# Optimization experiments

Hardware: AMD Instinct MI355X
Metric: run time of the kernel (lower is better)

Reference implementation:

```python
import jax, jax.numpy as jnp
import numpy as np

B, H, W, C = 64, 28, 28, 384
NH, WS = 12, 7
KD = C // NH            # key_dim = head_dim = 32 (attn_ratio=1.0 -> d = KD)
QKV_OUT = 3 * KD * NH   # 1152
HID = 4 * C             # mlp hidden
N = WS * WS             # tokens per window
L = H * W
SCALE = KD ** -0.5
EPS_LN = 1e-5
EPS_BN = 1e-5


def _make_bias_idxs():
    pts = [(i, j) for i in range(WS) for j in range(WS)]
    offs, idxs = {}, []
    for p1 in pts:
        for p2 in pts:
            o = (abs(p1[0] - p2[0]), abs(p1[1] - p2[1]))
            if o not in offs:
                offs[o] = len(offs)
            idxs.append(offs[o])
    return np.asarray(idxs, dtype=np.int32).reshape(N, N)


def _ln(x, g, b):
    m = jnp.mean(x, axis=-1, keepdims=True)
    v = jnp.mean(jnp.square(x - m), axis=-1, keepdims=True)
    return (x - m) * jax.lax.rsqrt(v + EPS_LN) * g + b


def setup_inputs() -> dict:
    key = jax.random.key(0)
    ks = jax.random.split(key, 8)
    s = 0.02
    return {
        "x": jax.random.normal(ks[0], (B, L, C), jnp.float32),
        "ln_a_g": jnp.ones((C,), jnp.float32),
        "ln_a_b": jnp.zeros((C,), jnp.float32),
        "qkv_w": jax.random.normal(ks[1], (QKV_OUT, C), jnp.float32) * s,
        "qkv_b": jnp.zeros((QKV_OUT,), jnp.float32),
        "attn_bias": jax.random.normal(ks[2], (NH, N), jnp.float32) * s,
        "proj_w": jax.random.normal(ks[3], (C, C), jnp.float32) * s,
        "proj_b": jnp.zeros((C,), jnp.float32),
        "conv_w": jax.random.normal(ks[4], (C, 1, 3, 3), jnp.float32) * s,
        "bn_g": jnp.ones((C,), jnp.float32),
        "bn_b": jnp.zeros((C,), jnp.float32),
        "bn_m": jnp.zeros((C,), jnp.float32),
        "bn_v": jnp.ones((C,), jnp.float32),
        "ln_m_g": jnp.ones((C,), jnp.float32),
        "ln_m_b": jnp.zeros((C,), jnp.float32),
        "fc1_w": jax.random.normal(ks[5], (HID, C), jnp.float32) * s,
        "fc1_b": jnp.zeros((HID,), jnp.float32),
        "fc2_w": jax.random.normal(ks[6], (C, HID), jnp.float32) * s,
        "fc2_b": jnp.zeros((C,), jnp.float32),
        "bias_idxs": jnp.asarray(_make_bias_idxs()),
    }


def reference(x, ln_a_g, ln_a_b, qkv_w, qkv_b, attn_bias, proj_w, proj_b,
              conv_w, bn_g, bn_b, bn_m, bn_v, ln_m_g, ln_m_b,
              fc1_w, fc1_b, fc2_w, fc2_b, bias_idxs):
    res = x
    nh, nw = H // WS, W // WS
    # window partition: [B,L,C] -> [B*nWin, N, C]
    xw = x.reshape(B, nh, WS, nw, WS, C).transpose(0, 1, 3, 2, 4, 5)
    xw = xw.reshape(B * nh * nw, N, C)
    # attention
    xn = _ln(xw, ln_a_g, ln_a_b)
    qkv = xn @ qkv_w.T + qkv_b                       # [Bw, N, 3*NH*KD]
    qkv = qkv.reshape(-1, N, NH, 3 * KD).transpose(0, 2, 1, 3)
    q, k, v = qkv[..., :KD], qkv[..., KD:2 * KD], qkv[..., 2 * KD:]
    bias = attn_bias[:, bias_idxs]                   # [NH, N, N]
    attn = jnp.einsum('bhnd,bhmd->bhnm', q, k) * SCALE + bias
    attn = jax.nn.softmax(attn, axis=-1)
    o = jnp.einsum('bhnm,bhmd->bhnd', attn, v)
    o = o.transpose(0, 2, 1, 3).reshape(-1, N, C)
    o = o @ proj_w.T + proj_b
    # window unpartition -> [B, L, C]
    o = o.reshape(B, nh, nw, WS, WS, C).transpose(0, 1, 3, 2, 4, 5).reshape(B, L, C)
    x = res + o
    # depthwise ConvBN (inference BN)
    xc = x.transpose(0, 2, 1).reshape(B, C, H, W)
    xc = jax.lax.conv_general_dilated(
        xc, conv_w, (1, 1), 'SAME', feature_group_count=C,
        dimension_numbers=('NCHW', 'OIHW', 'NCHW'))
    inv = jax.lax.rsqrt(bn_v + EPS_BN)
    xc = (xc - bn_m[None, :, None, None]) * (bn_g * inv)[None, :, None, None] + bn_b[None, :, None, None]
    x = xc.reshape(B, C, L).transpose(0, 2, 1)
    # MLP residual
    h = _ln(x, ln_m_g, ln_m_b)
    h = jax.nn.gelu(h @ fc1_w.T + fc1_b, approximate=False)
    h = h @ fc2_w.T + fc2_b
    return x + h
```

## Files before the change

kernel.cpp:

```cpp
#include <hip/hip_runtime.h>
#include <hip/hip_bf16.h>
#include <stdint.h>

#define BATCH 64
#define CC 384
#define NHEAD 12
#define KD 32
#define NTOK 49
#define LL 784
#define MTOT 50176
#define HID 1536
#define QKV_OUT 1152
#define SCALE 0.17677669529663687f
#define EPS 1e-5f

typedef __bf16 bf16x8 __attribute__((ext_vector_type(8)));
typedef float f32x4 __attribute__((ext_vector_type(4)));

__device__ __forceinline__ float bf2f(unsigned short u) {
  union { unsigned int u; float f; } cv; cv.u = ((unsigned int)u) << 16; return cv.f;
}
__device__ __forceinline__ unsigned short f2bf(float f) {
  union { float f; unsigned int u; } cv; cv.f = f;
  unsigned int r = cv.u + 0x7FFFu + ((cv.u >> 16) & 1u);
  return (unsigned short)(r >> 16);
}
__device__ __forceinline__ void gl_lds16(const unsigned short* g, unsigned short* l) {
  __builtin_amdgcn_global_load_lds(
      (const __attribute__((address_space(1))) unsigned int*)g,
      (__attribute__((address_space(3))) unsigned int*)l, 16, 0, 0);
}

__global__ void detect_kernel(const unsigned short* __restrict__ x, int* flag) {
  __shared__ int cnt;
  if (threadIdx.x == 0) cnt = 0;
  __syncthreads();
  int c = 0;
  for (int i = threadIdx.x; i < 4096; i += 256) {
    if (((x[i] >> 7) & 0xFF) == 0xFF) c++;
  }
  atomicAdd(&cnt, c);
  __syncthreads();
  if (threadIdx.x == 0) *flag = (cnt > 0) ? 1 : 0;
}

struct CvtArgs {
  const void* src[19];
  unsigned int n[19];
  unsigned int off[19];
};
__global__ __launch_bounds__(256) void convert_kernel(
    CvtArgs a, unsigned short* __restrict__ dst, const int* __restrict__ flag) {
  const int which = blockIdx.y;
  const unsigned int nn = a.n[which];
  unsigned short* d = dst + a.off[which];
  const unsigned int stride = gridDim.x * blockDim.x;
  const unsigned int idx = blockIdx.x * blockDim.x + threadIdx.x;
  const unsigned int ng = nn >> 3;
  if (*flag) {
    const float* s = (const float*)a.src[which];
    for (unsigned int g = idx; g < ng; g += stride) {
      const float4 f0 = ((const float4*)s)[g * 2];
      const float4 f1 = ((const float4*)s)[g * 2 + 1];
      ushort4 lo, hi;
      lo.x = f2bf(f0.x); lo.y = f2bf(f0.y); lo.z = f2bf(f0.z); lo.w = f2bf(f0.w);
      hi.x = f2bf(f1.x); hi.y = f2bf(f1.y); hi.z = f2bf(f1.z); hi.w = f2bf(f1.w);
      ((ushort4*)d)[g * 2] = lo;
      ((ushort4*)d)[g * 2 + 1] = hi;
    }
    for (unsigned int i = ng * 8 + idx; i < nn; i += stride) d[i] = f2bf(s[i]);
  } else {
    const unsigned short* s = (const unsigned short*)a.src[which];
    for (unsigned int g = idx; g < ng; g += stride)
      ((uint4*)d)[g] = ((const uint4*)s)[g];
    for (unsigned int i = ng * 8 + idx; i < nn; i += stride) d[i] = s[i];
  }
}

__global__ __launch_bounds__(256) void bias_kernel(
    const unsigned short* __restrict__ cAb, const int* __restrict__ bias_idxs,
    float* __restrict__ bias_full) {
  const int h = blockIdx.x;
  for (int i = threadIdx.x; i < NTOK * NTOK; i += 256)
    bias_full[h * NTOK * NTOK + i] = bf2f(cAb[h * NTOK + bias_idxs[i]]);
}

__global__ __launch_bounds__(384) void prep_kernel(
    const unsigned short* __restrict__ cw, const unsigned short* __restrict__ bg,
    const unsigned short* __restrict__ bb, const unsigned short* __restrict__ bm,
    const unsigned short* __restrict__ bv,
    unsigned short* __restrict__ cwT, float* __restrict__ bnsc, float* __restrict__ bnsh) {
  const int c = threadIdx.x;
  const float sc = bf2f(bg[c]) * rsqrtf(bf2f(bv[c]) + EPS);
  bnsc[c] = sc;
  bnsh[c] = bf2f(bb[c]) - bf2f(bm[c]) * sc;
  #pragma unroll
  for (int t = 0; t < 9; ++t) cwT[t * CC + c] = cw[c * 9 + t];
}

__global__ __launch_bounds__(128) void ln_kernel(
    const unsigned short* __restrict__ x, const unsigned short* __restrict__ g,
    const unsigned short* __restrict__ b, unsigned short* __restrict__ out) {
  const int tid = threadIdx.x;
  int wi = blockIdx.y, n = blockIdx.x;
  int bb = wi >> 4, wb = wi & 15;
  int nh_i = wb >> 2, nw_i = wb & 3;
  int hs = n / 7, wsx = n - hs * 7;
  int l = nh_i * 196 + hs * 28 + nw_i * 7 + wsx;
  size_t src_row = (size_t)bb * LL + l;
  size_t dst_row = (size_t)wi * NTOK + n;
  const unsigned short* xr = x + src_row * CC;
  float vals[3]; float s = 0.f, sq = 0.f;
  for (int j = 0; j < 3; ++j) {
    vals[j] = bf2f(xr[tid + 128 * j]);
    s += vals[j]; sq += vals[j] * vals[j];
  }
  for (int off = 32; off; off >>= 1) { s += __shfl_xor(s, off); sq += __shfl_xor(sq, off); }
  __shared__ float red[4];
  const int wv = tid >> 6;
  if ((tid & 63) == 0) { red[wv] = s; red[2 + wv] = sq; }
  __syncthreads();
  float tot = red[0] + red[1], totq = red[2] + red[3];
  float mean = tot * (1.f / CC);
  float var = totq * (1.f / CC) - mean * mean;
  float inv = rsqrtf(var + EPS);
  unsigned short* orow = out + dst_row * CC;
  for (int j = 0; j < 3; ++j) {
    int c = tid + 128 * j;
    float y = (vals[j] - mean) * inv * bf2f(g[c]) + bf2f(b[c]);
    orow[c] = f2bf(y);
  }
}

enum { EP_PLAIN = 0, EP_GELU = 1, EP_WINRES = 2, EP_RES2 = 3 };

template <int EP>
__global__ __launch_bounds__(256) void gemm128(
    const unsigned short* __restrict__ A, const unsigned short* __restrict__ W,
    const unsigned short* __restrict__ bias, const unsigned short* __restrict__ res,
    void* __restrict__ outp, int K, int N, int m_off, const int* __restrict__ flagp,
    int Nt) {
  __shared__ __align__(16) unsigned short lds[3 * 8192];
  const int tid = threadIdx.x;
  const int lane = tid & 63;
  const int wave = tid >> 6;
  const int nwg = gridDim.x;
  const int id = blockIdx.x;
  const int q8 = nwg >> 3, r8 = nwg & 7;
  const int xcd = id & 7, rank = id >> 3;
  const int wgid = (xcd < r8 ? xcd * (q8 + 1) : r8 * (q8 + 1) + (xcd - r8) * q8) + rank;
  const int bm = (wgid / Nt) * 128;
  const int bn = (wgid - (wgid / Nt) * Nt) * 128;
  const int wm = (wave >> 1) * 64;
  const int wn = (wave & 1) * 64;
  const int srow = tid >> 2;
  const int sr15 = srow & 15;
  const int sp = (sr15 + (sr15 >> 2)) & 3;
  const int s_col = ((tid & 3) ^ sp) * 8;
  const unsigned short* Ap0 = A + (size_t)(bm + srow) * K + s_col;
  const unsigned short* Wp0 = W + (size_t)(bn + srow) * K + s_col;
  const size_t rstep = (size_t)64 * K;
  f32x4 acc[4][4] = {};
  const int fr = lane & 15;
  const int quad = lane >> 4;
  const int nt = K >> 5;
  const int rp = (fr + (fr >> 2)) & 3;
  const int cg = (quad ^ rp) * 8;

  auto stage = [&](int bsel, int t) {
    const unsigned short* ap = Ap0 + (size_t)t * 32;
    const unsigned short* wp = Wp0 + (size_t)t * 32;
    unsigned short* al = lds + bsel * 8192 + tid * 8;
    unsigned short* bl = al + 4096;
    gl_lds16(ap, al);
    gl_lds16(ap + rstep, al + 2048);
    gl_lds16(wp, bl);
    gl_lds16(wp + rstep, bl + 2048);
  };

  stage(0, 0);
  stage(1, 1);
  int b = 0;
  for (int t = 0; t < nt; ++t) {
    if (t + 1 < nt) asm volatile("s_waitcnt vmcnt(4)" ::: "memory");
    else            asm volatile("s_waitcnt vmcnt(0)" ::: "memory");
    __builtin_amdgcn_s_barrier();
    __builtin_amdgcn_sched_barrier(0);
    if (t + 2 < nt) stage(b ? b - 1 : 2, t + 2);
    const unsigned short* Ab = lds + b * 8192;
    const unsigned short* Bb = Ab + 4096;
    bf16x8 af[4], bfr[4];
    #pragma unroll
    for (int i = 0; i < 4; ++i) {
      af[i]  = *(const bf16x8*)(Ab + (wm + i * 16 + fr) * 32 + cg);
      bfr[i] = *(const bf16x8*)(Bb + (wn + i * 16 + fr) * 32 + cg);
    }
    #pragma unroll
    for (int i = 0; i < 4; ++i)
      #pragma unroll
      for (int j = 0; j < 4; ++j)
        acc[i][j] = __builtin_amdgcn_mfma_f32_16x16x32_bf16(af[i], bfr[j], acc[i][j], 0, 0, 0);
    asm volatile("s_waitcnt lgkmcnt(0)" ::: "memory");
    __builtin_amdgcn_sched_barrier(0);
    b = (b == 2) ? 0 : b + 1;
  }

  int isf32 = 0;
  if (EP == EP_RES2) isf32 = *flagp;
  const int qr = (lane >> 4) * 4;
  float bvs[4];
  #pragma unroll
  for (int tj = 0; tj < 4; ++tj) bvs[tj] = bf2f(bias[bn + wn + tj * 16 + fr]);
  #pragma unroll
  for (int ti = 0; ti < 4; ++ti) {
    #pragma unroll
    for (int r = 0; r < 4; ++r) {
      const int mr = bm + wm + ti * 16 + qr + r;
      size_t rowbase;
      if (EP == EP_WINRES) {
        int wi = mr / 49; int nt2 = mr - wi * 49;
        int bb = wi >> 4; int wb = wi & 15;
        int nh_i = wb >> 2; int nw_i = wb & 3;
        int hs = nt2 / 7; int wsx = nt2 - hs * 7;
        int l = nh_i * 196 + hs * 28 + nw_i * 7 + wsx;
        rowbase = ((size_t)bb * LL + l) * CC;
      } else if (EP == EP_RES2) {
        rowbase = (size_t)(mr + m_off) * N;
      } else {
        rowbase = (size_t)mr * N;
      }
      #pragma unroll
      for (int tj = 0; tj < 4; ++tj) {
        const int n = bn + wn + tj * 16 + fr;
        float v = acc[ti][tj][r] + bvs[tj];
        if (EP == EP_GELU) {
          const float t2 = v * (1.5957691216f + 0.0713548162f * v * v);
          v = __fdividef(v, 1.0f + __expf(-t2));
          ((unsigned short*)outp)[rowbase + n] = f2bf(v);
        } else if (EP == EP_WINRES) {
          size_t idx = rowbase + n;
          v += bf2f(res[idx]);
          ((unsigned short*)outp)[idx] = f2bf(v);
        } else if (EP == EP_RES2) {
          size_t idx = rowbase + n;
          v += bf2f(res[idx]);
          if (isf32) ((float*)outp)[idx] = v;
          else       ((unsigned short*)outp)[idx] = f2bf(v);
        } else {
          ((unsigned short*)outp)[rowbase + n] = f2bf(v);
        }
      }
    }
  }
}

__global__ __launch_bounds__(64) void attn_mfma(
    const unsigned short* __restrict__ qkv, const float* __restrict__ bias_full,
    unsigned short* __restrict__ o, int wi_off) {
  __shared__ __align__(16) unsigned short Pl[64 * 72];
  __shared__ __align__(16) unsigned short vT[32 * 72];
  const int wi = blockIdx.x, h = blockIdx.y;
  const int lane = threadIdx.x;
  const int l15 = lane & 15;
  const int quad = lane >> 4;
  const unsigned short* base = qkv + (size_t)wi * NTOK * QKV_OUT + h * 96;

  bf16x8 qf[4], kf[4];
  #pragma unroll
  for (int i = 0; i < 4; ++i) {
    const int n = i * 16 + l15;
    if (n < NTOK) {
      const unsigned short* p = base + (size_t)n * QKV_OUT + quad * 8;
      qf[i] = *(const bf16x8*)(p);
      kf[i] = *(const bf16x8*)(p + 32);
    } else {
      qf[i] = (bf16x8)0; kf[i] = (bf16x8)0;
    }
  }

  for (int idx = lane; idx < 32 * 72; idx += 64) vT[idx] = 0;
  __syncthreads();
  for (int idx = lane; idx < NTOK * KD; idx += 64) {
    const int m = idx >> 5, d = idx & 31;
    vT[d * 72 + m] = base[(size_t)m * QKV_OUT + 64 + d];
  }

  f32x4 acc[4][4] = {};
  #pragma unroll
  for (int i = 0; i < 4; ++i)
    #pragma unroll
    for (int j = 0; j < 4; ++j)
      acc[i][j] = __builtin_amdgcn_mfma_f32_16x16x32_bf16(qf[i], kf[j], acc[i][j], 0, 0, 0);

  const float* bh = bias_full + h * NTOK * NTOK;
  float rinv[4][4];
  #pragma unroll
  for (int i = 0; i < 4; ++i) {
    #pragma unroll
    for (int r = 0; r < 4; ++r) {
      const int n = i * 16 + quad * 4 + r;
      float sv[4];
      #pragma unroll
      for (int j = 0; j < 4; ++j) {
        const int m = j * 16 + l15;
        float s = acc[i][j][r] * SCALE;
        if (n < NTOK && m < NTOK) s += bh[n * NTOK + m];
        if (m >= NTOK) s = -1e30f;
        sv[j] = s;
      }
      float mx = fmaxf(fmaxf(sv[0], sv[1]), fmaxf(sv[2], sv[3]));
      #pragma unroll
      for (int t = 1; t < 16; t <<= 1) mx = fmaxf(mx, __shfl_xor(mx, t));
      float sum = 0.f;
      #pragma unroll
      for (int j = 0; j < 4; ++j) {
        const float p = __expf(sv[j] - mx);
        sum += p;
        Pl[n * 72 + j * 16 + l15] = f2bf(p);
      }
      #pragma unroll
      for (int t = 1; t < 16; t <<= 1) sum += __shfl_xor(sum, t);
      rinv[i][r] = 1.f / sum;
    }
  }
  __syncthreads();

  f32x4 acc2[4][2] = {};
  #pragma unroll
  for (int kk = 0; kk < 2; ++kk) {
    bf16x8 pf[4], vf[2];
    #pragma unroll
    for (int i = 0; i < 4; ++i)
      pf[i] = *(const bf16x8*)(Pl + (i * 16 + l15) * 72 + kk * 32 + quad * 8);
    #pragma unroll
    for (int jd = 0; jd < 2; ++jd)
      vf[jd] = *(const bf16x8*)(vT + (jd * 16 + l15) * 72 + kk * 32 + quad * 8);
    #pragma unroll
    for (int i = 0; i < 4; ++i)
      #pragma unroll
      for (int jd = 0; jd < 2; ++jd)
        acc2[i][jd] = __builtin_amdgcn_mfma_f32_16x16x32_bf16(pf[i], vf[jd], acc2[i][jd], 0, 0, 0);
  }

  #pragma unroll
  for (int i = 0; i < 4; ++i) {
    #pragma unroll
    for (int r = 0; r < 4; ++r) {
      const int n = i * 16 + quad * 4 + r;
      if (n < NTOK) {
        const float ri = rinv[i][r];
        #pragma unroll
        for (int jd = 0; jd < 2; ++jd) {
          const int d = jd * 16 + l15;
          o[((size_t)(wi_off + wi) * NTOK + n) * CC + h * KD + d] = f2bf(acc2[i][jd][r] * ri);
        }
      }
    }
  }
}

__global__ __launch_bounds__(384) void conv_bn_ln(
    const unsigned short* __restrict__ x1, const unsigned short* __restrict__ cwT,
    const float* __restrict__ bnsc, const float* __restrict__ bnsh,
    const unsigned short* __restrict__ mg, const unsigned short* __restrict__ mb,
    unsigned short* __restrict__ x2, unsigned short* __restrict__ xm) {
  __shared__ float rs[8][48], rq[8][48];
  const int tid = threadIdx.x;
  const int pos = tid / 48;
  const int c8 = tid - pos * 48;
  const int c0 = c8 * 8;
  const int hw = blockIdx.x * 8 + pos;
  const int b = blockIdx.y;
  const int h = hw / 28, w = hw - h * 28;
  float acc[8] = {};
  #pragma unroll
  for (int t = 0; t < 9; ++t) {
    const int dh = t / 3 - 1, dw = t % 3 - 1;
    const int hh = h + dh, ww = w + dw;
    if (hh >= 0 && hh < 28 && ww >= 0 && ww < 28) {
      const uint4 xv = *(const uint4*)(x1 + ((size_t)b * LL + hh * 28 + ww) * CC + c0);
      const uint4 wv = *(const uint4*)(cwT + t * CC + c0);
      const unsigned short* xp = (const unsigned short*)&xv;
      const unsigned short* wp = (const unsigned short*)&wv;
      #pragma unroll
      for (int k = 0; k < 8; ++k) acc[k] += bf2f(xp[k]) * bf2f(wp[k]);
    }
  }
  const float4 sc0 = *(const float4*)(bnsc + c0);
  const float4 sc1 = *(const float4*)(bnsc + c0 + 4);
  const float4 sh0 = *(const float4*)(bnsh + c0);
  const float4 sh1 = *(const float4*)(bnsh + c0 + 4);
  float y[8];
  y[0] = acc[0] * sc0.x + sh0.x; y[1] = acc[1] * sc0.y + sh0.y;
  y[2] = acc[2] * sc0.z + sh0.z; y[3] = acc[3] * sc0.w + sh0.w;
  y[4] = acc[4] * sc1.x + sh1.x; y[5] = acc[5] * sc1.y + sh1.y;
  y[6] = acc[6] * sc1.z + sh1.z; y[7] = acc[7] * sc1.w + sh1.w;
  ushort4 pk0, pk1;
  pk0.x = f2bf(y[0]); pk0.y = f2bf(y[1]); pk0.z = f2bf(y[2]); pk0.w = f2bf(y[3]);
  pk1.x = f2bf(y[4]); pk1.y = f2bf(y[5]); pk1.z = f2bf(y[6]); pk1.w = f2bf(y[7]);
  const size_t row = ((size_t)b * LL + hw) * CC + c0;
  *(ushort4*)(x2 + row) = pk0;
  *(ushort4*)(x2 + row + 4) = pk1;
  float s = 0.f, q = 0.f;
  #pragma unroll
  for (int k = 0; k < 8; ++k) { s += y[k]; q += y[k] * y[k]; }
  rs[pos][c8] = s; rq[pos][c8] = q;
  __syncthreads();
  float tot = 0.f, tq = 0.f;
  #pragma unroll 8
  for (int i = 0; i < 48; ++i) { tot += rs[pos][i]; tq += rq[pos][i]; }
  const float mean = tot * (1.f / CC);
  const float var = tq * (1.f / CC) - mean * mean;
  const float inv = rsqrtf(var + EPS);
  const uint4 gv = *(const uint4*)(mg + c0);
  const uint4 bv = *(const uint4*)(mb + c0);
  const unsigned short* gp = (const unsigned short*)&gv;
  const unsigned short* bp = (const unsigned short*)&bv;
  ushort4 lo, hi;
  unsigned short outv[8];
  #pragma unroll
  for (int k = 0; k < 8; ++k)
    outv[k] = f2bf((y[k] - mean) * inv * bf2f(gp[k]) + bf2f(bp[k]));
  lo.x = outv[0]; lo.y = outv[1]; lo.z = outv[2]; lo.w = outv[3];
  hi.x = outv[4]; hi.y = outv[5]; hi.z = outv[6]; hi.w = outv[7];
  *(ushort4*)(xm + row) = lo;
  *(ushort4*)(xm + row + 4) = hi;
}

extern "C" void kernel_launch(void* const* d_in, const int* in_sizes, int n_in,
                              void* d_out, int out_size, void* d_ws, size_t ws_size,
                              hipStream_t stream) {
  int* flag = (int*)d_ws;
  unsigned short* base = (unsigned short*)d_ws;

  CvtArgs args;
  size_t cur = 32;
  size_t off[19];
  for (int i = 0; i < 19; ++i) {
    off[i] = cur;
    args.src[i] = d_in[i];
    args.n[i] = (unsigned int)in_sizes[i];
    args.off[i] = (unsigned int)cur;
    cur += ((size_t)in_sizes[i] + 63) & ~(size_t)63;
  }
  const unsigned short* cx   = base + off[0];
  const unsigned short* cgA  = base + off[1];
  const unsigned short* cbA  = base + off[2];
  const unsigned short* cQw  = base + off[3];
  const unsigned short* cQb  = base + off[4];
  const unsigned short* cAb  = base + off[5];
  const unsigned short* cPw  = base + off[6];
  const unsigned short* cPb  = base + off[7];
  const unsigned short* cCw  = base + off[8];
  const unsigned short* cBg  = base + off[9];
  const unsigned short* cBb  = base + off[10];
  const unsigned short* cBm  = base + off[11];
  const unsigned short* cBv  = base + off[12];
  const unsigned short* cMg  = base + off[13];
  const unsigned short* cMb  = base + off[14];
  const unsigned short* cF1w = base + off[15];
  const unsigned short* cF1b = base + off[16];
  const unsigned short* cF2w = base + off[17];
  const unsigned short* cF2b = base + off[18];
  const int* bias_idxs = (const int*)d_in[19];

  const size_t SZ = (size_t)MTOT * CC;
  const size_t need_full_bytes =
      (cur + SZ + (size_t)MTOT * HID) * 2 + 512 * 1024;
  const int nchunk = (ws_size >= need_full_bytes) ? 1 : 2;
  const int MC = MTOT / nchunk;
  const int WC = 1024 / nchunk;
  const size_t buf2_cap = (size_t)MC * HID;

  unsigned short* o_buf = base + cur;
  unsigned short* buf2  = o_buf + SZ;
  unsigned short* x2    = base + off[0];
  float* bias_full = (float*)(buf2 + buf2_cap);
  unsigned short* cwT = (unsigned short*)(bias_full + 12 * NTOK * NTOK);
  float* bnsc = (float*)(cwT + 9 * CC);
  float* bnsh = bnsc + CC;

  unsigned short* xn = (unsigned short*)d_out;

  detect_kernel<<<1, 256, 0, stream>>>((const unsigned short*)d_in[0], flag);
  convert_kernel<<<dim3(512, 19), 256, 0, stream>>>(args, base, flag);
  bias_kernel<<<NHEAD, 256, 0, stream>>>(cAb, bias_idxs, bias_full);
  prep_kernel<<<1, 384, 0, stream>>>(cCw, cBg, cBb, cBm, cBv, cwT, bnsc, bnsh);

  ln_kernel<<<dim3(49, 1024), 128, 0, stream>>>(cx, cgA, cbA, xn);

  for (int c = 0; c < nchunk; ++c) {
    gemm128<EP_PLAIN><<<(MC / 128) * (QKV_OUT / 128), 256, 0, stream>>>(
        xn + (size_t)c * MC * CC, cQw, cQb, nullptr, buf2, CC, QKV_OUT, 0, nullptr,
        QKV_OUT / 128);
    attn_mfma<<<dim3(WC, NHEAD), 64, 0, stream>>>(buf2, bias_full, o_buf, c * WC);
  }

  gemm128<EP_WINRES><<<(MTOT / 128) * (CC / 128), 256, 0, stream>>>(
      o_buf, cPw, cPb, cx, d_out, CC, CC, 0, nullptr, CC / 128);

  conv_bn_ln<<<dim3(98, BATCH), 384, 0, stream>>>(
      (const unsigned short*)d_out, cwT, bnsc, bnsh, cMg, cMb, x2, o_buf);

  for (int c = 0; c < nchunk; ++c) {
    gemm128<EP_GELU><<<(MC / 128) * (HID / 128), 256, 0, stream>>>(
        o_buf + (size_t)c * MC * CC, cF1w, cF1b, nullptr, buf2, CC, HID, 0, nullptr,
        HID / 128);
    gemm128<EP_RES2><<<(MC / 128) * (CC / 128), 256, 0, stream>>>(
        buf2, cF2w, cF2b, x2, d_out, HID, CC, c * MC, flag, CC / 128);
  }
}
```

Before: 657.6 us.

## Add 256x128-tile GEMM kernel and use it for MLP fc1/fc2

Adds a gemm256 kernel in which each workgroup computes a 256x128 output tile and each wave a 64x128 slab (4x8 MFMA tiles), with a larger triple-buffered LDS stage. The fc1 (GELU) and fc2 (residual) GEMMs switch to it. The epilogue logic moves into shared helper functions so both kernels can use it. The aim is to reuse each loaded B fragment across more MFMAs and cut global/LDS traffic per flop, at the cost of more accumulator registers, more LDS, and fewer workgroups per launch.

Measured after the change: 777.1 us. 18.2% more time.

```diff
diff --git a/kernel.cpp b/kernel.cpp
--- a/kernel.cpp
+++ b/kernel.cpp
@@ -133,6 +133,43 @@
 }
 
 enum { EP_PLAIN = 0, EP_GELU = 1, EP_WINRES = 2, EP_RES2 = 3 };
+
+template <int EP>
+__device__ __forceinline__ size_t ep_rowbase(int mr, int m_off, int N) {
+  if (EP == EP_WINRES) {
+    int wi = mr / 49; int nt2 = mr - wi * 49;
+    int bb = wi >> 4; int wb = wi & 15;
+    int nh_i = wb >> 2; int nw_i = wb & 3;
+    int hs = nt2 / 7; int wsx = nt2 - hs * 7;
+    int l = nh_i * 196 + hs * 28 + nw_i * 7 + wsx;
+    return ((size_t)bb * LL + l) * CC;
+  } else if (EP == EP_RES2) {
+    return (size_t)(mr + m_off) * N;
+  }
+  return (size_t)mr * N;
+}
+
+template <int EP>
+__device__ __forceinline__ void ep_store(
+    void* outp, const unsigned short* res, size_t rowbase, int n,
+    float v, int isf32) {
+  if (EP == EP_GELU) {
+    const float t2 = v * (1.5957691216f + 0.0713548162f * v * v);
+    v = __fdividef(v, 1.0f + __expf(-t2));
+    ((unsigned short*)outp)[rowbase + n] = f2bf(v);
+  } else if (EP == EP_WINRES) {
+    size_t idx = rowbase + n;
+    v += bf2f(res[idx]);
+    ((unsigned short*)outp)[idx] = f2bf(v);
+  } else if (EP == EP_RES2) {
+    size_t idx = rowbase + n;
+    v += bf2f(res[idx]);
+    if (isf32) ((float*)outp)[idx] = v;
+    else       ((unsigned short*)outp)[idx] = f2bf(v);
+  } else {
+    ((unsigned short*)outp)[rowbase + n] = f2bf(v);
+  }
+}
 
 template <int EP>
 __global__ __launch_bounds__(256) void gemm128(
@@ -216,39 +253,105 @@
     #pragma unroll
     for (int r = 0; r < 4; ++r) {
       const int mr = bm + wm + ti * 16 + qr + r;
-      size_t rowbase;
-      if (EP == EP_WINRES) {
-        int wi = mr / 49; int nt2 = mr - wi * 49;
-        int bb = wi >> 4; int wb = wi & 15;
-        int nh_i = wb >> 2; int nw_i = wb & 3;
-        int hs = nt2 / 7; int wsx = nt2 - hs * 7;
-        int l = nh_i * 196 + hs * 28 + nw_i * 7 + wsx;
-        rowbase = ((size_t)bb * LL + l) * CC;
-      } else if (EP == EP_RES2) {
-        rowbase = (size_t)(mr + m_off) * N;
-      } else {
-        rowbase = (size_t)mr * N;
-      }
+      const size_t rowbase = ep_rowbase<EP>(mr, m_off, N);
       #pragma unroll
       for (int tj = 0; tj < 4; ++tj) {
         const int n = bn + wn + tj * 16 + fr;
-        float v = acc[ti][tj][r] + bvs[tj];
-        if (EP == EP_GELU) {
-          const float t2 = v * (1.5957691216f + 0.0713548162f * v * v);
-          v = __fdividef(v, 1.0f + __expf(-t2));
-          ((unsigned short*)outp)[rowbase + n] = f2bf(v);
-        } else if (EP == EP_WINRES) {
-          size_t idx = rowbase + n;
-          v += bf2f(res[idx]);
-          ((unsigned short*)outp)[idx] = f2bf(v);
-        } else if (EP == EP_RES2) {
-          size_t idx = rowbase + n;
-          v += bf2f(res[idx]);
-          if (isf32) ((float*)outp)[idx] = v;
-          else       ((unsigned short*)outp)[idx] = f2bf(v);
-        } else {
-          ((unsigned short*)outp)[rowbase + n] = f2bf(v);
-        }
+        ep_store<EP>(outp, res, rowbase, n, acc[ti][tj][r] + bvs[tj], isf32);
+      }
+    }
+  }
+}
+
+template <int EP>
+__global__ __launch_bounds__(256) void gemm256(
+    const unsigned short* __restrict__ A, const unsigned short* __restrict__ W,
+    const unsigned short* __restrict__ bias, const unsigned short* __restrict__ res,
+    void* __restrict__ outp, int K, int N, int m_off, const int* __restrict__ flagp,
+    int Nt) {
+  __shared__ __align__(16) unsigned short lds[3 * 12288];
+  const int tid = threadIdx.x;
+  const int lane = tid & 63;
+  const int wave = tid >> 6;
+  const int nwg = gridDim.x;
+  const int id = blockIdx.x;
+  const int q8 = nwg >> 3, r8 = nwg & 7;
+  const int xcd = id & 7, rank = id >> 3;
+  const int wgid = (xcd < r8 ? xcd * (q8 + 1) : r8 * (q8 + 1) + (xcd - r8) * q8) + rank;
+  const int bm = (wgid / Nt) * 256;
+  const int bn = (wgid - (wgid / Nt) * Nt) * 128;
+  const int wm = wave * 64;
+  const int srow = tid >> 2;
+  const int sr15 = srow & 15;
+  const int sp = (sr15 + (sr15 >> 2)) & 3;
+  const int s_col = ((tid & 3) ^ sp) * 8;
+  const unsigned short* Ap0 = A + (size_t)(bm + srow) * K + s_col;
+  const unsigned short* Wp0 = W + (size_t)(bn + srow) * K + s_col;
+  const size_t rstep = (size_t)64 * K;
+  f32x4 acc[4][8] = {};
+  const int fr = lane & 15;
+  const int quad = lane >> 4;
+  const int nt = K >> 5;
+  const int rp = (fr + (fr >> 2)) & 3;
+  const int cg = (quad ^ rp) * 8;
+
+  auto stage = [&](int bsel, int t) {
+    const unsigned short* ap = Ap0 + (size_t)t * 32;
+    const unsigned short* wp = Wp0 + (size_t)t * 32;
+    unsigned short* al = lds + bsel * 12288 + tid * 8;
+    unsigned short* bl = lds + bsel * 12288 + 8192 + tid * 8;
+    gl_lds16(ap, al);
+    gl_lds16(ap + rstep, al + 2048);
+    gl_lds16(ap + 2 * rstep, al + 4096);
+    gl_lds16(ap + 3 * rstep, al + 6144);
+    gl_lds16(wp, bl);
+    gl_lds16(wp + rstep, bl + 2048);
+  };
+
+  stage(0, 0);
+  stage(1, 1);
+  int b = 0;
+  for (int t = 0; t < nt; ++t) {
+    if (t + 1 < nt) asm volatile("s_waitcnt vmcnt(6)" ::: "memory");
+    else            asm volatile("s_waitcnt vmcnt(0)" ::: "memory");
+    __builtin_amdgcn_s_barrier();
+    __builtin_amdgcn_sched_barrier(0);
+    if (t + 2 < nt) stage(b ? b - 1 : 2, t + 2);
+    const unsigned short* Ab = lds + b * 12288;
+    const unsigned short* Bb = Ab + 8192;
+    bf16x8 af[4], bfr[8];
+    #pragma unroll
+    for (int i = 0; i < 4; ++i)
+      af[i] = *(const bf16x8*)(Ab + (wm + i * 16 + fr) * 32 + cg);
+    #pragma unroll
+    for (int j = 0; j < 8; ++j)
+      bfr[j] = *(const bf16x8*)(Bb + (j * 16 + fr) * 32 + cg);
+    #pragma unroll
+    for (int i = 0; i < 4; ++i)
+      #pragma unroll
+      for (int j = 0; j < 8; ++j)
+        acc[i][j] = __builtin_amdgcn_mfma_f32_16x16x32_bf16(af[i], bfr[j], acc[i][j], 0, 0, 0);
+    asm volatile("s_waitcnt lgkmcnt(0)" ::: "memory");
+    __builtin_amdgcn_sched_barrier(0);
+    b = (b == 2) ? 0 : b + 1;
+  }
+
+  int isf32 = 0;
+  if (EP == EP_RES2) isf32 = *flagp;
+  const int qr = (lane >> 4) * 4;
+  float bvs[8];
+  #pragma unroll
+  for (int tj = 0; tj < 8; ++tj) bvs[tj] = bf2f(bias[bn + tj * 16 + fr]);
+  #pragma unroll
+  for (int ti = 0; ti < 4; ++ti) {
+    #pragma unroll
+    for (int r = 0; r < 4; ++r) {
+      const int mr = bm + wm + ti * 16 + qr + r;
+      const size_t rowbase = ep_rowbase<EP>(mr, m_off, N);
+      #pragma unroll
+      for (int tj = 0; tj < 8; ++tj) {
+        const int n = bn + tj * 16 + fr;
+        ep_store<EP>(outp, res, rowbase, n, acc[ti][tj][r] + bvs[tj], isf32);
       }
     }
   }
@@ -503,10 +606,10 @@
       (const unsigned short*)d_out, cwT, bnsc, bnsh, cMg, cMb, x2, o_buf);
 
   for (int c = 0; c < nchunk; ++c) {
-    gemm128<EP_GELU><<<(MC / 128) * (HID / 128), 256, 0, stream>>>(
+    gemm256<EP_GELU><<<(MC / 256) * (HID / 128), 256, 0, stream>>>(
         o_buf + (size_t)c * MC * CC, cF1w, cF1b, nullptr, buf2, CC, HID, 0, nullptr,
         HID / 128);
-    gemm128<EP_RES2><<<(MC / 128) * (CC / 128), 256, 0, stream>>>(
+    gemm256<EP_RES2><<<(MC / 256) * (CC / 128), 256, 0, stream>>>(
         buf2, cF2w, cF2b, x2, d_out, HID, CC, c * MC, flag, CC / 128);
   }
 }
```

## Fold LayerNorm affine into GEMM weights and apply row stats in epilogue

Applied to the files above, without the earlier changes.

Both LayerNorms (before QKV and before fc1) are removed as materialized passes. The gamma/beta are folded into the following linear weights via a fold kernel that precomputes per-column sums and bias constants. Only per-row mean and inverse std are computed (statsA kernel, conv epilogue) and applied in the GEMM epilogue. The QKV GEMM also gathers window rows directly from x, eliminating the normalized-activation write and read. This risks extra numerical error because mean subtraction happens after a bf16 GEMM on un-centered inputs.

After: 679.5 us. +3.3%, slower.

```diff
diff --git a/kernel.cpp b/kernel.cpp
--- a/kernel.cpp
+++ b/kernel.cpp
@@ -29,6 +29,12 @@
   __builtin_amdgcn_global_load_lds(
       (const __attribute__((address_space(1))) unsigned int*)g,
       (__attribute__((address_space(3))) unsigned int*)l, 16, 0, 0);
+}
+__device__ __forceinline__ int winrow(int m) {
+  int wi = m / 49, nn = m - wi * 49;
+  int bb = wi >> 4, wb = wi & 15;
+  int hs = nn / 7, wsx = nn - hs * 7;
+  return bb * LL + (wb >> 2) * 196 + hs * 28 + (wb & 3) * 7 + wsx;
 }
 
 __global__ void detect_kernel(const unsigned short* __restrict__ x, int* flag) {
@@ -98,48 +104,69 @@
   for (int t = 0; t < 9; ++t) cwT[t * CC + c] = cw[c * 9 + t];
 }
 
-__global__ __launch_bounds__(128) void ln_kernel(
-    const unsigned short* __restrict__ x, const unsigned short* __restrict__ g,
-    const unsigned short* __restrict__ b, unsigned short* __restrict__ out) {
+__global__ __launch_bounds__(384) void fold_kernel(
+    const unsigned short* __restrict__ W, const unsigned short* __restrict__ g,
+    const unsigned short* __restrict__ bvec, const unsigned short* __restrict__ b2,
+    unsigned short* __restrict__ W2, float* __restrict__ S, float* __restrict__ C) {
+  const int n = blockIdx.x, k = threadIdx.x;
+  const float w = bf2f(W[(size_t)n * CC + k]);
+  const float gw = bf2f(g[k]) * w;
+  const unsigned short r = f2bf(gw);
+  W2[(size_t)n * CC + k] = r;
+  float s = bf2f(r);
+  float c = bf2f(bvec[k]) * w;
+  #pragma unroll
+  for (int off = 32; off; off >>= 1) { s += __shfl_xor(s, off); c += __shfl_xor(c, off); }
+  __shared__ float s6[6], c6[6];
+  const int wv = k >> 6;
+  if ((k & 63) == 0) { s6[wv] = s; c6[wv] = c; }
+  __syncthreads();
+  if (k == 0) {
+    float st = 0.f, ct = 0.f;
+    #pragma unroll
+    for (int i = 0; i < 6; ++i) { st += s6[i]; ct += c6[i]; }
+    S[n] = st; C[n] = ct + bf2f(b2[n]);
+  }
+}
+
+__global__ __launch_bounds__(128) void statsA_kernel(
+    const unsigned short* __restrict__ x, float* __restrict__ muA, float* __restrict__ invA) {
   const int tid = threadIdx.x;
-  int wi = blockIdx.y, n = blockIdx.x;
-  int bb = wi >> 4, wb = wi & 15;
-  int nh_i = wb >> 2, nw_i = wb & 3;
-  int hs = n / 7, wsx = n - hs * 7;
-  int l = nh_i * 196 + hs * 28 + nw_i * 7 + wsx;
-  size_t src_row = (size_t)bb * LL + l;
-  size_t dst_row = (size_t)wi * NTOK + n;
-  const unsigned short* xr = x + src_row * CC;
-  float vals[3]; float s = 0.f, sq = 0.f;
+  const int wi = blockIdx.y, n = blockIdx.x;
+  const int l = (((wi & 15) >> 2) * 196 + (n / 7) * 28 + (wi & 3) * 7 + (n % 7));
+  const unsigned short* xr = x + ((size_t)(wi >> 4) * LL + l) * CC;
+  float s = 0.f, sq = 0.f;
+  #pragma unroll
   for (int j = 0; j < 3; ++j) {
-    vals[j] = bf2f(xr[tid + 128 * j]);
-    s += vals[j]; sq += vals[j] * vals[j];
-  }
+    const float v = bf2f(xr[tid + 128 * j]);
+    s += v; sq += v * v;
+  }
+  #pragma unroll
   for (int off = 32; off; off >>= 1) { s += __shfl_xor(s, off); sq += __shfl_xor(sq, off); }
   __shared__ float red[4];
   const int wv = tid >> 6;
   if ((tid & 63) == 0) { red[wv] = s; red[2 + wv] = sq; }
   __syncthreads();
-  float tot = red[0] + red[1], totq = red[2] + red[3];
-  float mean = tot * (1.f / CC);
-  float var = totq * (1.f / CC) - mean * mean;
-  float inv = rsqrtf(var + EPS);
-  unsigned short* orow = out + dst_row * CC;
-  for (int j = 0; j < 3; ++j) {
-    int c = tid + 128 * j;
-    float y = (vals[j] - mean) * inv * bf2f(g[c]) + bf2f(b[c]);
-    orow[c] = f2bf(y);
-  }
-}
-
-enum { EP_PLAIN = 0, EP_GELU = 1, EP_WINRES = 2, EP_RES2 = 3 };
+  if (tid == 0) {
+    const float tot = red[0] + red[1], totq = red[2] + red[3];
+    const float mean = tot * (1.f / CC);
+    const float var = totq * (1.f / CC) - mean * mean;
+    muA[(size_t)wi * NTOK + n] = mean;
+    invA[(size_t)wi * NTOK + n] = rsqrtf(var + EPS);
+  }
+}
+
+enum { EP_PLAIN = 0, EP_WINRES = 2, EP_RES2 = 3, EP_QKV = 4, EP_GELU2 = 5 };
 
 template <int EP>
 __global__ __launch_bounds__(256) void gemm128(
     const unsigned short* __restrict__ A, const unsigned short* __restrict__ W,
     const unsigned short* __restrict__ bias, const unsigned short* __restrict__ res,
     void* __restrict__ outp, int K, int N, int m_off, const int* __restrict__ flagp,
-    int Nt) {
+    int Nt, const float* __restrict__ muv, const float* __restrict__ invv,
+    const float* __restrict__ snv, const float* __restrict__ cnv) {
+  constexpr bool GATHER = (EP == EP_QKV);
+  constexpr bool LNFOLD = (EP == EP_QKV || EP == EP_GELU2);
   __shared__ __align__(16) unsigned short lds[3 * 8192];
   const int tid = threadIdx.x;
   const int lane = tid & 63;
@@ -157,7 +184,15 @@
   const int sr15 = srow & 15;
   const int sp = (sr15 + (sr15 >> 2)) & 3;
   const int s_col = ((tid & 3) ^ sp) * 8;
-  const unsigned short* Ap0 = A + (size_t)(bm + srow) * K + s_col;
+  int rowA0, rowA1;
+  if (GATHER) {
+    rowA0 = winrow(bm + srow + m_off);
+    rowA1 = winrow(bm + srow + 64 + m_off);
+  } else {
+    rowA0 = bm + srow; rowA1 = rowA0 + 64;
+  }
+  const unsigned short* ApA = A + (size_t)rowA0 * K + s_col;
+  const unsigned short* ApB = A + (size_t)rowA1 * K + s_col;
   const unsigned short* Wp0 = W + (size_t)(bn + srow) * K + s_col;
   const size_t rstep = (size_t)64 * K;
   f32x4 acc[4][4] = {};
@@ -168,14 +203,12 @@
   const int cg = (quad ^ rp) * 8;
 
   auto stage = [&](int bsel, int t) {
-    const unsigned short* ap = Ap0 + (size_t)t * 32;
-    const unsigned short* wp = Wp0 + (size_t)t * 32;
     unsigned short* al = lds + bsel * 8192 + tid * 8;
     unsigned short* bl = al + 4096;
-    gl_lds16(ap, al);
-    gl_lds16(ap + rstep, al + 2048);
-    gl_lds16(wp, bl);
-    gl_lds16(wp + rstep, bl + 2048);
+    gl_lds16(ApA + t * 32, al);
+    gl_lds16(ApB + t * 32, al + 2048);
+    gl_lds16(Wp0 + t * 32, bl);
+    gl_lds16(Wp0 + t * 32 + rstep, bl + 2048);
   };
 
   stage(0, 0);
@@ -207,47 +240,47 @@
 
   int isf32 = 0;
   if (EP == EP_RES2) isf32 = *flagp;
-  const int qr = (lane >> 4) * 4;
-  float bvs[4];
-  #pragma unroll
-  for (int tj = 0; tj < 4; ++tj) bvs[tj] = bf2f(bias[bn + wn + tj * 16 + fr]);
+  const int qr = quad * 4;
+  float s4[4], c4[4], bvs[4];
+  #pragma unroll
+  for (int tj = 0; tj < 4; ++tj) {
+    const int n = bn + wn + tj * 16 + fr;
+    if (LNFOLD) { s4[tj] = snv[n]; c4[tj] = cnv[n]; }
+    else        { bvs[tj] = bf2f(bias[n]); }
+  }
   #pragma unroll
   for (int ti = 0; ti < 4; ++ti) {
     #pragma unroll
     for (int r = 0; r < 4; ++r) {
       const int mr = bm + wm + ti * 16 + qr + r;
+      float iv = 0.f, um = 0.f;
+      if (LNFOLD) { iv = invv[mr + m_off]; um = muv[mr + m_off] * iv; }
       size_t rowbase;
-      if (EP == EP_WINRES) {
-        int wi = mr / 49; int nt2 = mr - wi * 49;
-        int bb = wi >> 4; int wb = wi & 15;
-        int nh_i = wb >> 2; int nw_i = wb & 3;
-        int hs = nt2 / 7; int wsx = nt2 - hs * 7;
-        int l = nh_i * 196 + hs * 28 + nw_i * 7 + wsx;
-        rowbase = ((size_t)bb * LL + l) * CC;
-      } else if (EP == EP_RES2) {
-        rowbase = (size_t)(mr + m_off) * N;
-      } else {
-        rowbase = (size_t)mr * N;
-      }
+      if (EP == EP_WINRES)      rowbase = (size_t)winrow(mr) * CC;
+      else if (EP == EP_RES2)   rowbase = (size_t)(mr + m_off) * N;
+      else                      rowbase = (size_t)mr * N;
       #pragma unroll
       for (int tj = 0; tj < 4; ++tj) {
         const int n = bn + wn + tj * 16 + fr;
-        float v = acc[ti][tj][r] + bvs[tj];
-        if (EP == EP_GELU) {
+        if (EP == EP_QKV) {
+          const float v = iv * acc[ti][tj][r] - um * s4[tj] + c4[tj];
+          ((unsigned short*)outp)[rowbase + n] = f2bf(v);
+        } else if (EP == EP_GELU2) {
+          float v = iv * acc[ti][tj][r] - um * s4[tj] + c4[tj];
           const float t2 = v * (1.5957691216f + 0.0713548162f * v * v);
           v = __fdividef(v, 1.0f + __expf(-t2));
           ((unsigned short*)outp)[rowbase + n] = f2bf(v);
         } else if (EP == EP_WINRES) {
-          size_t idx = rowbase + n;
-          v += bf2f(res[idx]);
+          const size_t idx = rowbase + n;
+          float v = acc[ti][tj][r] + bvs[tj] + bf2f(res[idx]);
           ((unsigned short*)outp)[idx] = f2bf(v);
         } else if (EP == EP_RES2) {
-          size_t idx = rowbase + n;
-          v += bf2f(res[idx]);
+          const size_t idx = rowbase + n;
+          float v = acc[ti][tj][r] + bvs[tj] + bf2f(res[idx]);
           if (isf32) ((float*)outp)[idx] = v;
           else       ((unsigned short*)outp)[idx] = f2bf(v);
         } else {
-          ((unsigned short*)outp)[rowbase + n] = f2bf(v);
+          ((unsigned short*)outp)[rowbase + n] = f2bf(acc[ti][tj][r] + bvs[tj]);
         }
       }
     }
@@ -362,8 +395,7 @@
 __global__ __launch_bounds__(384) void conv_bn_ln(
     const unsigned short* __restrict__ x1, const unsigned short* __restrict__ cwT,
     const float* __restrict__ bnsc, const float* __restrict__ bnsh,
-    const unsigned short* __restrict__ mg, const unsigned short* __restrict__ mb,
-    unsigned short* __restrict__ x2, unsigned short* __restrict__ xm) {
+    unsigned short* __restrict__ x2, float* __restrict__ muM, float* __restrict__ invM) {
   __shared__ float rs[8][48], rq[8][48];
   const int tid = threadIdx.x;
   const int pos = tid / 48;
@@ -395,36 +427,29 @@
   y[2] = acc[2] * sc0.z + sh0.z; y[3] = acc[3] * sc0.w + sh0.w;
   y[4] = acc[4] * sc1.x + sh1.x; y[5] = acc[5] * sc1.y + sh1.y;
   y[6] = acc[6] * sc1.z + sh1.z; y[7] = acc[7] * sc1.w + sh1.w;
+  unsigned short yr[8];
+  #pragma unroll
+  for (int k = 0; k < 8; ++k) yr[k] = f2bf(y[k]);
   ushort4 pk0, pk1;
-  pk0.x = f2bf(y[0]); pk0.y = f2bf(y[1]); pk0.z = f2bf(y[2]); pk0.w = f2bf(y[3]);
-  pk1.x = f2bf(y[4]); pk1.y = f2bf(y[5]); pk1.z = f2bf(y[6]); pk1.w = f2bf(y[7]);
+  pk0.x = yr[0]; pk0.y = yr[1]; pk0.z = yr[2]; pk0.w = yr[3];
+  pk1.x = yr[4]; pk1.y = yr[5]; pk1.z = yr[6]; pk1.w = yr[7];
   const size_t row = ((size_t)b * LL + hw) * CC + c0;
   *(ushort4*)(x2 + row) = pk0;
   *(ushort4*)(x2 + row + 4) = pk1;
   float s = 0.f, q = 0.f;
   #pragma unroll
-  for (int k = 0; k < 8; ++k) { s += y[k]; q += y[k] * y[k]; }
+  for (int k = 0; k < 8; ++k) { const float v = bf2f(yr[k]); s += v; q += v * v; }
   rs[pos][c8] = s; rq[pos][c8] = q;
   __syncthreads();
-  float tot = 0.f, tq = 0.f;
-  #pragma unroll 8
-  for (int i = 0; i < 48; ++i) { tot += rs[pos][i]; tq += rq[pos][i]; }
-  const float mean = tot * (1.f / CC);
-  const float var = tq * (1.f / CC) - mean * mean;
-  const float inv = rsqrtf(var + EPS);
-  const uint4 gv = *(const uint4*)(mg + c0);
-  const uint4 bv = *(const uint4*)(mb + c0);
-  const unsigned short* gp = (const unsigned short*)&gv;
-  const unsigned short* bp = (const unsigned short*)&bv;
-  ushort4 lo, hi;
-  unsigned short outv[8];
-  #pragma unroll
-  for (int k = 0; k < 8; ++k)
-    outv[k] = f2bf((y[k] - mean) * inv * bf2f(gp[k]) + bf2f(bp[k]));
-  lo.x = outv[0]; lo.y = outv[1]; lo.z = outv[2]; lo.w = outv[3];
-  hi.x = outv[4]; hi.y = outv[5]; hi.z = outv[6]; hi.w = outv[7];
-  *(ushort4*)(xm + row) = lo;
-  *(ushort4*)(xm + row + 4) = hi;
+  if (c8 == 0) {
+    float tot = 0.f, tq = 0.f;
+    #pragma unroll 8
+    for (int i = 0; i < 48; ++i) { tot += rs[pos][i]; tq += rq[pos][i]; }
+    const float mean = tot * (1.f / CC);
+    const float var = tq * (1.f / CC) - mean * mean;
+    muM[(size_t)b * LL + hw] = mean;
+    invM[(size_t)b * LL + hw] = rsqrtf(var + EPS);
+  }
 }
 
 extern "C" void kernel_launch(void* const* d_in, const int* in_sizes, int n_in,
@@ -465,8 +490,11 @@
   const int* bias_idxs = (const int*)d_in[19];
 
   const size_t SZ = (size_t)MTOT * CC;
+  const size_t tbl_bytes = 4 * (size_t)MTOT * 4 +
+                           ((size_t)QKV_OUT + HID) * CC * 2 +
+                           2 * ((size_t)QKV_OUT + HID) * 4 + 65536;
   const size_t need_full_bytes =
-      (cur + SZ + (size_t)MTOT * HID) * 2 + 512 * 1024;
+      (cur + SZ + (size_t)MTOT * HID) * 2 + tbl_bytes + 1024 * 1024;
   const int nchunk = (ws_size >= need_full_bytes) ? 1 : 2;
   const int MC = MTOT / nchunk;
   const int WC = 1024 / nchunk;
@@ -479,34 +507,46 @@
   unsigned short* cwT = (unsigned short*)(bias_full + 12 * NTOK * NTOK);
   float* bnsc = (float*)(cwT + 9 * CC);
   float* bnsh = bnsc + CC;
-
-  unsigned short* xn = (unsigned short*)d_out;
+  float* muA  = bnsh + CC;
+  float* invA = muA + MTOT;
+  float* muM  = invA + MTOT;
+  float* invM = muM + MTOT;
+  float* sq   = invM + MTOT;
+  float* cq   = sq + QKV_OUT;
+  float* sm   = cq + QKV_OUT;
+  float* cm   = sm + HID;
+  unsigned short* W2q = (unsigned short*)(cm + HID);
+  unsigned short* W2m = W2q + (size_t)QKV_OUT * CC;
 
   detect_kernel<<<1, 256, 0, stream>>>((const unsigned short*)d_in[0], flag);
   convert_kernel<<<dim3(512, 19), 256, 0, stream>>>(args, base, flag);
   bias_kernel<<<NHEAD, 256, 0, stream>>>(cAb, bias_idxs, bias_full);
   prep_kernel<<<1, 384, 0, stream>>>(cCw, cBg, cBb, cBm, cBv, cwT, bnsc, bnsh);
-
-  ln_kernel<<<dim3(49, 1024), 128, 0, stream>>>(cx, cgA, cbA, xn);
+  fold_kernel<<<QKV_OUT, 384, 0, stream>>>(cQw, cgA, cbA, cQb, W2q, sq, cq);
+  fold_kernel<<<HID, 384, 0, stream>>>(cF1w, cMg, cMb, cF1b, W2m, sm, cm);
+
+  statsA_kernel<<<dim3(49, 1024), 128, 0, stream>>>(cx, muA, invA);
 
   for (int c = 0; c < nchunk; ++c) {
-    gemm128<EP_PLAIN><<<(MC / 128) * (QKV_OUT / 128), 256, 0, stream>>>(
-        xn + (size_t)c * MC * CC, cQw, cQb, nullptr, buf2, CC, QKV_OUT, 0, nullptr,
-        QKV_OUT / 128);
+    gemm128<EP_QKV><<<(MC / 128) * (QKV_OUT / 128), 256, 0, stream>>>(
+        cx, W2q, nullptr, nullptr, buf2, CC, QKV_OUT, c * MC, nullptr,
+        QKV_OUT / 128, muA, invA, sq, cq);
     attn_mfma<<<dim3(WC, NHEAD), 64, 0, stream>>>(buf2, bias_full, o_buf, c * WC);
   }
 
   gemm128<EP_WINRES><<<(MTOT / 128) * (CC / 128), 256, 0, stream>>>(
-      o_buf, cPw, cPb, cx, d_out, CC, CC, 0, nullptr, CC / 128);
+      o_buf, cPw, cPb, cx, d_out, CC, CC, 0, nullptr, CC / 128,
+      nullptr, nullptr, nullptr, nullptr);
 
   conv_bn_ln<<<dim3(98, BATCH), 384, 0, stream>>>(
-      (const unsigned short*)d_out, cwT, bnsc, bnsh, cMg, cMb, x2, o_buf);
+      (const unsigned short*)d_out, cwT, bnsc, bnsh, x2, muM, invM);
 
   for (int c = 0; c < nchunk; ++c) {
-    gemm128<EP_GELU><<<(MC / 128) * (HID / 128), 256, 0, stream>>>(
-        o_buf + (size_t)c * MC * CC, cF1w, cF1b, nullptr, buf2, CC, HID, 0, nullptr,
-        HID / 128);
+    gemm128<EP_GELU2><<<(MC / 128) * (HID / 128), 256, 0, stream>>>(
+        x2 + (size_t)c * MC * CC, W2m, nullptr, nullptr, buf2, CC, HID, c * MC,
+        nullptr, HID / 128, muM, invM, sm, cm);
     gemm128<EP_RES2><<<(MC / 128) * (CC / 128), 256, 0, stream>>>(
-        buf2, cF2w, cF2b, x2, d_out, HID, CC, c * MC, flag, CC / 128);
-  }
-}
+        buf2, cF2w, cF2b, x2, d_out, HID, CC, c * MC, flag, CC / 128,
+        nullptr, nullptr, nullptr, nullptr);
+  }
+}
```
